# Optimization experiments

Measured on AMD Instinct MI355X. Metric: run time of the kernel, lower is better.

Reference implementation:

```python
import jax, jax.numpy as jnp
import numpy as np

B, NP, K = 8, 512, 64   # graphs, points per graph, knn neighbors
N = B * NP              # total nodes
EPS = 1e-5


def knn_edges(pos):
    """knn_graph(pos, k=K, batch, loop=True): edges (src=j neighbor, dst=i)."""
    p = pos.reshape(B, NP, 3)
    d2 = jnp.sum((p[:, :, None, :] - p[:, None, :, :]) ** 2, axis=-1)  # [B,NP,NP]
    _, idx = jax.lax.top_k(-d2, K)  # [B,NP,K] nearest (self included, d2=0)
    off = (jnp.arange(B, dtype=jnp.int32) * NP)[:, None, None]
    src = (idx.astype(jnp.int32) + off).reshape(-1)
    dst = jnp.broadcast_to(jnp.arange(NP, dtype=jnp.int32)[None, :, None] + off,
                           (B, NP, K)).reshape(-1)
    return src, dst


def graph_norm(x, batch, w, b, ms):
    """PyG GraphNorm: per-graph mean/std with learnable mean scale."""
    cnt = jax.ops.segment_sum(jnp.ones((x.shape[0], 1), x.dtype), batch, B)
    mean = jax.ops.segment_sum(x, batch, B) / cnt
    out = x - mean[batch] * ms
    var = jax.ops.segment_sum(out * out, batch, B) / cnt
    return w * out / jnp.sqrt(var + EPS)[batch] + b


def pointnet_layer(h, pos, src, dst, w1, b1, w2, b2):
    """message = MLP(concat(h_j, pos_j - pos_i)); aggregate = scatter-max over dst."""
    m = jnp.concatenate([h[src], pos[src] - pos[dst]], axis=-1)  # [E, Cin+3]
    m = jax.nn.relu(m @ w1 + b1) @ w2 + b2                        # [E, Cout]
    return jax.ops.segment_max(m, dst, N)


def _forward(batch, pos,
             gn1_w, gn1_b, gn1_ms, gn2_w, gn2_b, gn2_ms, gn3_w, gn3_b, gn3_ms,
             gn4_w, gn4_b, gn4_ms, gn5_w, gn5_b, gn5_ms, gn6_w, gn6_b, gn6_ms,
             c1_w1, c1_b1, c1_w2, c1_b2, c2_w1, c2_b1, c2_w2, c2_b2,
             c3_w1, c3_b1, c3_w2, c3_b2, c4_w1, c4_b1, c4_w2, c4_b2,
             c5_w1, c5_b1, c5_w2, c5_b2, cls_w, cls_b):
    src, dst = knn_edges(pos)
    h = graph_norm(pos, batch, gn1_w, gn1_b, gn1_ms)
    h = pointnet_layer(h, pos, src, dst, c1_w1, c1_b1, c1_w2, c1_b2)
    h = jax.nn.relu(graph_norm(h, batch, gn2_w, gn2_b, gn2_ms))
    h = pointnet_layer(h, pos, src, dst, c2_w1, c2_b1, c2_w2, c2_b2)
    h = jax.nn.relu(graph_norm(h, batch, gn3_w, gn3_b, gn3_ms))
    h = pointnet_layer(h, pos, src, dst, c3_w1, c3_b1, c3_w2, c3_b2)
    h = jax.nn.relu(graph_norm(h, batch, gn4_w, gn4_b, gn4_ms))
    h = pointnet_layer(h, pos, src, dst, c4_w1, c4_b1, c4_w2, c4_b2)
    h = jax.nn.relu(graph_norm(h, batch, gn5_w, gn5_b, gn5_ms))
    h = pointnet_layer(h, pos, src, dst, c5_w1, c5_b1, c5_w2, c5_b2)
    h = jax.nn.relu(graph_norm(h, batch, gn6_w, gn6_b, gn6_ms))
    return h @ cls_w + cls_b  # [N, 14]


def setup_inputs() -> dict:
    key = jax.random.key(0)
    ks = iter(jax.random.split(key, 40))
    inp = {}
    inp["pos"] = jax.random.normal(next(ks), (N, 3), jnp.float32)
    inp["batch"] = jnp.repeat(jnp.arange(B, dtype=jnp.int32), NP)
    for i, c in enumerate([3, 64, 128, 256, 512, 512], 1):
        inp[f"gn{i}_w"] = jnp.ones((c,), jnp.float32)
        inp[f"gn{i}_b"] = jnp.zeros((c,), jnp.float32)
        inp[f"gn{i}_ms"] = jnp.ones((c,), jnp.float32)
    for i, (ci, co) in enumerate([(3, 64), (64, 128), (128, 256), (256, 512), (512, 512)], 1):
        fin = ci + 3
        inp[f"c{i}_w1"] = jax.random.normal(next(ks), (fin, co), jnp.float32) / np.sqrt(fin).astype(np.float32)
        inp[f"c{i}_b1"] = jnp.zeros((co,), jnp.float32)
        inp[f"c{i}_w2"] = jax.random.normal(next(ks), (co, co), jnp.float32) / np.sqrt(co).astype(np.float32)
        inp[f"c{i}_b2"] = jnp.zeros((co,), jnp.float32)
    inp["cls_w"] = jax.random.normal(next(ks), (512, 14), jnp.float32) / np.float32(np.sqrt(512))
    inp["cls_b"] = jnp.zeros((14,), jnp.float32)
    return inp


def reference(pos, batch,
              gn1_w, gn1_b, gn1_ms, gn2_w, gn2_b, gn2_ms, gn3_w, gn3_b, gn3_ms,
              gn4_w, gn4_b, gn4_ms, gn5_w, gn5_b, gn5_ms, gn6_w, gn6_b, gn6_ms,
              c1_w1, c1_b1, c1_w2, c1_b2, c2_w1, c2_b1, c2_w2, c2_b2,
              c3_w1, c3_b1, c3_w2, c3_b2, c4_w1, c4_b1, c4_w2, c4_b2,
              c5_w1, c5_b1, c5_w2, c5_b2, cls_w, cls_b):
    return _forward(batch, pos,
                    gn1_w, gn1_b, gn1_ms, gn2_w, gn2_b, gn2_ms, gn3_w, gn3_b, gn3_ms,
                    gn4_w, gn4_b, gn4_ms, gn5_w, gn5_b, gn5_ms, gn6_w, gn6_b, gn6_ms,
                    c1_w1, c1_b1, c1_w2, c1_b2, c2_w1, c2_b1, c2_w2, c2_b2,
                    c3_w1, c3_b1, c3_w2, c3_b2, c4_w1, c4_b1, c4_w2, c4_b2,
                    c5_w1, c5_b1, c5_w2, c5_b2, cls_w, cls_b)
```

## Files before the change

kernel.cpp:

```cpp
#include <hip/hip_runtime.h>
#include <stdint.h>

#define N_NODES 4096
#define NGRAPH 8
#define NPTS 512
#define KNN 64
#define EPSN 1e-5f

typedef _Float16 f16x8 __attribute__((ext_vector_type(8)));
typedef float f32x4 __attribute__((ext_vector_type(4)));
typedef unsigned long long u64;

__device__ __forceinline__ unsigned short f2h(float f) {
    _Float16 h = (_Float16)f;
    union { _Float16 h; unsigned short u; } cv; cv.h = h;
    return cv.u;
}

__device__ __forceinline__ void w2cv(const float* __restrict__ src, unsigned short* __restrict__ dst,
                                     int off, int lg2c) {
    int C = 1 << lg2c;
    int k = off >> lg2c, n = off & (C - 1);
    int d = ((n >> 4) * (C / 32) + (k >> 5)) * 512 + ((k >> 3) & 3) * 128 + (n & 15) * 8 + (k & 7);
    dst[d] = f2h(src[off]);
}

__global__ __launch_bounds__(64) void setup_kernel(const float* __restrict__ pos, int* __restrict__ knn_out,
                                                   const float* __restrict__ wa, const float* __restrict__ wb,
                                                   const float* __restrict__ wc, const float* __restrict__ wd,
                                                   const float* __restrict__ we,
                                                   unsigned short* __restrict__ oa, unsigned short* __restrict__ ob,
                                                   unsigned short* __restrict__ oc, unsigned short* __restrict__ od,
                                                   unsigned short* __restrict__ oe,
                                                   float* __restrict__ statz,
                                                   const float* __restrict__ ms1, const float* __restrict__ gw1,
                                                   float* __restrict__ Aa, float* __restrict__ Sa) {
#pragma clang fp contract(off)
    __shared__ float px[NPTS], py[NPTS], pz[NPTS];
    __shared__ u64 keys[NPTS];
    int bid = blockIdx.x;
    int tid = threadIdx.x;
    int gidx = bid * 64 + tid;
    for (int idx = gidx; idx < 40960; idx += 262144) statz[idx] = 0.f;
    for (int idx = gidx; idx < 610304; idx += 262144) {
        if (idx < 4096)        w2cv(wa, oa, idx, 6);
        else if (idx < 20480)  w2cv(wb, ob, idx - 4096, 7);
        else if (idx < 86016)  w2cv(wc, oc, idx - 20480, 8);
        else if (idx < 348160) w2cv(wd, od, idx - 86016, 9);
        else                   w2cv(we, oe, idx - 348160, 9);
    }
    if (bid < 24) {
        int g = bid / 3, ch = bid - g * 3;
        float s1 = 0.f, s2 = 0.f;
        for (int n = tid; n < NPTS; n += 64) {
            float v = pos[(g * NPTS + n) * 3 + ch];
            s1 += v; s2 += v * v;
        }
        #pragma unroll
        for (int off = 32; off; off >>= 1) { s1 += __shfl_xor(s1, off); s2 += __shfl_xor(s2, off); }
        if (tid == 0) {
            float mean = s1 * (1.f / NPTS);
            float av = mean * ms1[ch];
            float var = s2 * (1.f / NPTS) - 2.f * av * mean + av * av;
            Aa[g * 3 + ch] = av;
            Sa[g * 3 + ch] = gw1[ch] / sqrtf(var + EPSN);
        }
    }
    int b = bid >> 9;
    int il = bid & (NPTS - 1);
    for (int n = tid; n < NPTS; n += 64) {
        int base = (b * NPTS + n) * 3;
        px[n] = pos[base]; py[n] = pos[base + 1]; pz[n] = pos[base + 2];
    }
    __syncthreads();
    float xi = px[il], yi = py[il], zi = pz[il];
    for (int n = tid; n < NPTS; n += 64) {
        float dx = px[n] - xi, dy = py[n] - yi, dz = pz[n] - zi;
        float d2 = dx * dx;
        d2 = d2 + dy * dy;
        d2 = d2 + dz * dz;
        keys[n] = (((u64)__float_as_uint(d2)) << 32) | (unsigned)n;
    }
    __syncthreads();
    for (int k2 = 2; k2 <= NPTS; k2 <<= 1) {
        for (int j = k2 >> 1; j > 0; j >>= 1) {
            #pragma unroll 4
            for (int p = 0; p < 4; ++p) {
                int pid = tid + p * 64;
                int t = ((pid & ~(j - 1)) << 1) | (pid & (j - 1));
                int ixj = t | j;
                u64 a = keys[t], c = keys[ixj];
                bool up = ((t & k2) == 0);
                if ((a > c) == up) { keys[t] = c; keys[ixj] = a; }
            }
            __syncthreads();
        }
    }
    int j0 = (int)(keys[tid] & 0xffffffffu);
    knn_out[(size_t)(b * NPTS + il) * KNN + tid] = b * NPTS + j0;
}

template<int CIN, int C, int RELU, int RAW>
__global__ __launch_bounds__(C) void node_kernel(const float* __restrict__ y, const float* __restrict__ pos,
                                                 const float* __restrict__ p1, const float* __restrict__ p2,
                                                 const float* __restrict__ ms, const float* __restrict__ gw,
                                                 const float* __restrict__ bnp,
                                                 const float* __restrict__ w1, const float* __restrict__ b1,
                                                 float* __restrict__ U, float* __restrict__ P) {
    constexpr int ROWS = 16;
    constexpr int KC = 64;
    constexpr int LDH = KC + 4;
    __shared__ float hs[ROWS][LDH];
    __shared__ float As_[CIN > 0 ? CIN : 1], Ss_[CIN > 0 ? CIN : 1];
    const int c = threadIdx.x;
    const int n0 = blockIdx.x * ROWS;
    const int b = n0 >> 9;
    if (RAW) {
        for (int ch = c; ch < CIN; ch += C) {
            float s1 = p1[b * CIN + ch], s2 = p2[b * CIN + ch];
            float mean = s1 * (1.f / NPTS);
            float a = mean * ms[ch];
            float var = s2 * (1.f / NPTS) - 2.f * a * mean + a * a;
            As_[ch] = a;
            Ss_[ch] = gw[ch] / sqrtf(var + EPSN);
        }
    }
    float acc[ROWS];
    #pragma unroll
    for (int r = 0; r < ROWS; ++r) acc[r] = 0.f;
    constexpr int NCHUNK = (CIN + KC - 1) / KC;
    #pragma unroll 1
    for (int s = 0; s < NCHUNK; ++s) {
        const int k0 = s * KC;
        const int kc = (CIN - k0 < KC) ? (CIN - k0) : KC;
        __syncthreads();
        for (int idx = c; idx < ROWS * kc; idx += C) {
            int r = idx / kc, k = idx - r * kc;
            int ch = k0 + k;
            float a = RAW ? As_[ch] : p1[b * CIN + ch];
            float sf = RAW ? Ss_[ch] : p2[b * CIN + ch];
            float v = (y[(size_t)(n0 + r) * CIN + ch] - a) * sf + bnp[ch];
            if (RELU) v = fmaxf(v, 0.f);
            hs[r][k] = v;
        }
        __syncthreads();
        int k = 0;
        for (; k + 4 <= kc; k += 4) {
            float w0 = w1[(size_t)(k0 + k) * C + c];
            float w1v = w1[(size_t)(k0 + k + 1) * C + c];
            float w2v = w1[(size_t)(k0 + k + 2) * C + c];
            float w3v = w1[(size_t)(k0 + k + 3) * C + c];
            #pragma unroll
            for (int r = 0; r < ROWS; ++r) {
                f32x4 hv = *(const f32x4*)&hs[r][k];
                acc[r] = fmaf(hv[0], w0, acc[r]);
                acc[r] = fmaf(hv[1], w1v, acc[r]);
                acc[r] = fmaf(hv[2], w2v, acc[r]);
                acc[r] = fmaf(hv[3], w3v, acc[r]);
            }
        }
        for (; k < kc; ++k) {
            float wv = w1[(size_t)(k0 + k) * C + c];
            #pragma unroll
            for (int r = 0; r < ROWS; ++r)
                acc[r] = fmaf(hs[r][k], wv, acc[r]);
        }
    }
    float pacc[ROWS];
    #pragma unroll
    for (int r = 0; r < ROWS; ++r) pacc[r] = 0.f;
    #pragma unroll
    for (int e = 0; e < 3; ++e) {
        float wv = w1[(size_t)(CIN + e) * C + c];
        #pragma unroll
        for (int r = 0; r < ROWS; ++r)
            pacc[r] = fmaf(pos[(n0 + r) * 3 + e], wv, pacc[r]);
    }
    float bv = b1[c];
    #pragma unroll
    for (int r = 0; r < ROWS; ++r) {
        U[(size_t)(n0 + r) * C + c] = acc[r] + pacc[r] + bv;
        P[(size_t)(n0 + r) * C + c] = pacc[r];
    }
}

template<int C, int W>
__global__ __launch_bounds__(W * 64, 4) void edge_kernel(const float* __restrict__ U, const float* __restrict__ P,
                                                         const int* __restrict__ knn, const unsigned short* __restrict__ w2t,
                                                         const float* __restrict__ b2, float* __restrict__ Y,
                                                         float* __restrict__ sum1, float* __restrict__ sum2) {
    constexpr int NCT = C / (W * 16);
    constexpr int EPT = 32 / W;
    constexpr int S = C / 32;
    constexpr int LD = 40;
    __shared__ unsigned short Tb[2][64 * LD];
    __shared__ int jn[64];
    const int bid = blockIdx.x;
    const int i = ((bid & 7) << 9) | (bid >> 3);
    const int tid = threadIdx.x;
    const int wave = tid >> 6, lane = tid & 63, m = lane & 15, quad = lane >> 4;
    const int cw = wave * (NCT * 16);
    if (tid < 64) jn[tid] = knn[(size_t)i * KNN + tid];
    f32x4 acc[4][NCT];
    f32x4 zero = {0.f, 0.f, 0.f, 0.f};
    #pragma unroll
    for (int rt = 0; rt < 4; ++rt)
        #pragma unroll
        for (int ct = 0; ct < NCT; ++ct)
            acc[rt][ct] = zero;
    const int rr = tid / W;
    const int c0 = (tid % W) * EPT;
    __syncthreads();
    const float* upr = U + (size_t)jn[rr] * C + c0;
    const float* ppr = P + (size_t)i * C + c0;
    float4 uf[EPT / 4], pf[EPT / 4];
    #pragma unroll
    for (int g = 0; g < EPT / 4; ++g) {
        uf[g] = *(const float4*)(upr + g * 4);
        pf[g] = *(const float4*)(ppr + g * 4);
    }
    #pragma unroll 2
    for (int s = 0; s < S; ++s) {
        unsigned short* tb = Tb[s & 1];
        if constexpr (EPT == 8) {
            uint4 pk;
            pk.x = (unsigned)f2h(fmaxf(uf[0].x - pf[0].x, 0.f)) | ((unsigned)f2h(fmaxf(uf[0].y - pf[0].y, 0.f)) << 16);
            pk.y = (unsigned)f2h(fmaxf(uf[0].z - pf[0].z, 0.f)) | ((unsigned)f2h(fmaxf(uf[0].w - pf[0].w, 0.f)) << 16);
            pk.z = (unsigned)f2h(fmaxf(uf[1].x - pf[1].x, 0.f)) | ((unsigned)f2h(fmaxf(uf[1].y - pf[1].y, 0.f)) << 16);
            pk.w = (unsigned)f2h(fmaxf(uf[1].z - pf[1].z, 0.f)) | ((unsigned)f2h(fmaxf(uf[1].w - pf[1].w, 0.f)) << 16);
            *(uint4*)&tb[rr * LD + c0] = pk;
        } else {
            uint2 pk;
            pk.x = (unsigned)f2h(fmaxf(uf[0].x - pf[0].x, 0.f)) | ((unsigned)f2h(fmaxf(uf[0].y - pf[0].y, 0.f)) << 16);
            pk.y = (unsigned)f2h(fmaxf(uf[0].z - pf[0].z, 0.f)) | ((unsigned)f2h(fmaxf(uf[0].w - pf[0].w, 0.f)) << 16);
            *(uint2*)&tb[rr * LD + c0] = pk;
        }
        if (s + 1 < S) {
            #pragma unroll
            for (int g = 0; g < EPT / 4; ++g) {
                uf[g] = *(const float4*)(upr + (s + 1) * 32 + g * 4);
                pf[g] = *(const float4*)(ppr + (s + 1) * 32 + g * 4);
            }
        }
        __syncthreads();
        f16x8 a[4];
        #pragma unroll
        for (int rt = 0; rt < 4; ++rt)
            a[rt] = *(const f16x8*)&tb[(rt * 16 + m) * LD + quad * 8];
        #pragma unroll
        for (int ct = 0; ct < NCT; ++ct) {
            const f16x8 bb = *(const f16x8*)(w2t +
                (size_t)(((cw >> 4) + ct) * S + s) * 512 + quad * 128 + m * 8);
            #pragma unroll
            for (int rt = 0; rt < 4; ++rt)
                acc[rt][ct] = __builtin_amdgcn_mfma_f32_16x16x32_f16(a[rt], bb, acc[rt][ct], 0, 0, 0);
        }
    }
    const int gb = i >> 9;
    #pragma unroll
    for (int ct = 0; ct < NCT; ++ct) {
        float vmax = -3.4e38f;
        #pragma unroll
        for (int rt = 0; rt < 4; ++rt) {
            vmax = fmaxf(vmax, acc[rt][ct][0]);
            vmax = fmaxf(vmax, acc[rt][ct][1]);
            vmax = fmaxf(vmax, acc[rt][ct][2]);
            vmax = fmaxf(vmax, acc[rt][ct][3]);
        }
        vmax = fmaxf(vmax, __shfl_xor(vmax, 16));
        vmax = fmaxf(vmax, __shfl_xor(vmax, 32));
        if (quad == 0) {
            int col = cw + ct * 16 + m;
            float val = vmax + b2[col];
            Y[(size_t)i * C + col] = val;
            atomicAdd(&sum1[gb * C + col], val);
            atomicAdd(&sum2[gb * C + col], val * val);
        }
    }
}

__global__ __launch_bounds__(256) void cls_kernel(const float* __restrict__ y, const float* __restrict__ sum1,
                                                  const float* __restrict__ sum2, const float* __restrict__ ms,
                                                  const float* __restrict__ gw, const float* __restrict__ gnb,
                                                  const float* __restrict__ w, const float* __restrict__ bias,
                                                  float* __restrict__ out) {
    __shared__ float wl[512 * 14];
    __shared__ _Float16 hn[16][520];
    __shared__ float As[512], Ss[512];
    int tid = threadIdx.x;
    int n0 = blockIdx.x * 16;
    int b = n0 >> 9;
    for (int ch = tid; ch < 512; ch += 256) {
        float s1 = sum1[b * 512 + ch], s2 = sum2[b * 512 + ch];
        float mean = s1 * (1.f / NPTS);
        float a = mean * ms[ch];
        float var = s2 * (1.f / NPTS) - 2.f * a * mean + a * a;
        As[ch] = a;
        Ss[ch] = gw[ch] / sqrtf(var + EPSN);
    }
    for (int idx = tid; idx < 512 * 14; idx += 256) wl[idx] = w[idx];
    __syncthreads();
    for (int idx = tid; idx < 16 * 512; idx += 256) {
        int r = idx >> 9, k = idx & 511;
        float v = (y[(size_t)(n0 + r) * 512 + k] - As[k]) * Ss[k] + gnb[k];
        hn[r][k] = (_Float16)fmaxf(v, 0.f);
    }
    __syncthreads();
    if (tid < 224) {
        int nl = tid / 14, c = tid - nl * 14;
        float acc = bias[c];
        for (int k = 0; k < 512; ++k)
            acc += (float)hn[nl][k] * wl[k * 14 + c];
        out[(size_t)(n0 + nl) * 14 + c] = acc;
    }
}

extern "C" void kernel_launch(void* const* d_in, const int* in_sizes, int n_in,
                              void* d_out, int out_size, void* d_ws, size_t ws_size,
                              hipStream_t stream) {
    const float* pos = (const float*)d_in[0];
    const float* gnw[6]; const float* gnb[6]; const float* gnms[6];
    for (int i = 0; i < 6; ++i) {
        gnw[i]  = (const float*)d_in[2 + 3 * i];
        gnb[i]  = (const float*)d_in[3 + 3 * i];
        gnms[i] = (const float*)d_in[4 + 3 * i];
    }
    const float* cw1[5]; const float* cb1[5]; const float* cw2[5]; const float* cb2[5];
    for (int i = 0; i < 5; ++i) {
        cw1[i] = (const float*)d_in[20 + 4 * i];
        cb1[i] = (const float*)d_in[21 + 4 * i];
        cw2[i] = (const float*)d_in[22 + 4 * i];
        cb2[i] = (const float*)d_in[23 + 4 * i];
    }
    const float* clsw = (const float*)d_in[40];
    const float* clsb = (const float*)d_in[41];
    float* out = (float*)d_out;

    char* ws = (char*)d_ws;
    int* knn             = (int*)(ws + 0);
    float* U             = (float*)(ws + 1048576);
    float* P             = (float*)(ws + 9437184);
    float* y             = (float*)(ws + 26214400);
    float* Aa            = (float*)(ws + 34603008);
    float* Sa            = (float*)(ws + 34619392);
    unsigned short* w2t0 = (unsigned short*)(ws + 34635776);
    unsigned short* w2t1 = (unsigned short*)(ws + 34643968);
    unsigned short* w2t2 = (unsigned short*)(ws + 34676736);
    unsigned short* w2t3 = (unsigned short*)(ws + 34807808);
    unsigned short* w2t4 = (unsigned short*)(ws + 35332096);
    float* acc           = (float*)(ws + 35856384);
    float* s1l[5]; float* s2l[5];
    for (int l = 0; l < 5; ++l) { s1l[l] = acc + l * 8192; s2l[l] = s1l[l] + 4096; }

    setup_kernel<<<N_NODES, 64, 0, stream>>>(pos, knn, cw2[0], cw2[1], cw2[2], cw2[3], cw2[4],
                                             w2t0, w2t1, w2t2, w2t3, w2t4, acc,
                                             gnms[0], gnw[0], Aa, Sa);

    node_kernel<3, 64, 0, 0><<<N_NODES / 16, 64, 0, stream>>>(pos, pos, Aa, Sa, gnms[0], gnw[0], gnb[0], cw1[0], cb1[0], U, P);
    edge_kernel<64, 4><<<N_NODES, 256, 0, stream>>>(U, P, knn, w2t0, cb2[0], y, s1l[0], s2l[0]);

    node_kernel<64, 128, 1, 1><<<N_NODES / 16, 128, 0, stream>>>(y, pos, s1l[0], s2l[0], gnms[1], gnw[1], gnb[1], cw1[1], cb1[1], U, P);
    edge_kernel<128, 8><<<N_NODES, 512, 0, stream>>>(U, P, knn, w2t1, cb2[1], y, s1l[1], s2l[1]);

    node_kernel<128, 256, 1, 1><<<N_NODES / 16, 256, 0, stream>>>(y, pos, s1l[1], s2l[1], gnms[2], gnw[2], gnb[2], cw1[2], cb1[2], U, P);
    edge_kernel<256, 8><<<N_NODES, 512, 0, stream>>>(U, P, knn, w2t2, cb2[2], y, s1l[2], s2l[2]);

    node_kernel<256, 512, 1, 1><<<N_NODES / 16, 512, 0, stream>>>(y, pos, s1l[2], s2l[2], gnms[3], gnw[3], gnb[3], cw1[3], cb1[3], U, P);
    edge_kernel<512, 8><<<N_NODES, 512, 0, stream>>>(U, P, knn, w2t3, cb2[3], y, s1l[3], s2l[3]);

    node_kernel<512, 512, 1, 1><<<N_NODES / 16, 512, 0, stream>>>(y, pos, s1l[3], s2l[3], gnms[4], gnw[4], gnb[4], cw1[4], cb1[4], U, P);
    edge_kernel<512, 8><<<N_NODES, 512, 0, stream>>>(U, P, knn, w2t4, cb2[4], y, s1l[4], s2l[4]);

    cls_kernel<<<N_NODES / 16, 256, 0, stream>>>(y, s1l[4], s2l[4], gnms[5], gnw[5], gnb[5], clsw, clsb, out);
}
```

Measured before the change: 749.2 us.

## Use 32x32x16 MFMA edge kernel with matching weight layout for wide layers

Adds an edge kernel built on 32x32x16 f16 MFMA tiles for the 256- and 512-channel layers, with a new swizzled weight layout produced in setup. It stages the relu(U_j - P_i) tile in double-buffered LDS in 32-wide K chunks and reduces the max over the 32-row accumulators. Larger MFMA tiles are meant to cut instruction count and LDS or global weight reads per FLOP. In exchange, the 16-float accumulators raise register pressure under launch bounds of 512 threads with 4 blocks per CU.

```diff
diff --git a/kernel.cpp b/kernel.cpp
--- a/kernel.cpp
+++ b/kernel.cpp
@@ -9,6 +9,7 @@
 
 typedef _Float16 f16x8 __attribute__((ext_vector_type(8)));
 typedef float f32x4 __attribute__((ext_vector_type(4)));
+typedef float f32x16 __attribute__((ext_vector_type(16)));
 typedef unsigned long long u64;
 
 __device__ __forceinline__ unsigned short f2h(float f) {
@@ -22,6 +23,13 @@
     int C = 1 << lg2c;
     int k = off >> lg2c, n = off & (C - 1);
     int d = ((n >> 4) * (C / 32) + (k >> 5)) * 512 + ((k >> 3) & 3) * 128 + (n & 15) * 8 + (k & 7);
+    dst[d] = f2h(src[off]);
+}
+__device__ __forceinline__ void w2cv32(const float* __restrict__ src, unsigned short* __restrict__ dst,
+                                       int off, int lg2c) {
+    int C = 1 << lg2c;
+    int k = off >> lg2c, n = off & (C - 1);
+    int d = ((n >> 5) * (C / 16) + (k >> 4)) * 512 + ((k >> 3) & 1) * 256 + (n & 31) * 8 + (k & 7);
     dst[d] = f2h(src[off]);
 }
 
@@ -45,9 +53,9 @@
     for (int idx = gidx; idx < 610304; idx += 262144) {
         if (idx < 4096)        w2cv(wa, oa, idx, 6);
         else if (idx < 20480)  w2cv(wb, ob, idx - 4096, 7);
-        else if (idx < 86016)  w2cv(wc, oc, idx - 20480, 8);
-        else if (idx < 348160) w2cv(wd, od, idx - 86016, 9);
-        else                   w2cv(we, oe, idx - 348160, 9);
+        else if (idx < 86016)  w2cv32(wc, oc, idx - 20480, 8);
+        else if (idx < 348160) w2cv32(wd, od, idx - 86016, 9);
+        else                   w2cv32(we, oe, idx - 348160, 9);
     }
     if (bid < 24) {
         int g = bid / 3, ch = bid - g * 3;
@@ -279,6 +287,89 @@
     }
 }
 
+template<int C>
+__global__ __launch_bounds__(512, 4) void edge_kernel32(const float* __restrict__ U, const float* __restrict__ P,
+                                                        const int* __restrict__ knn, const unsigned short* __restrict__ w2t,
+                                                        const float* __restrict__ b2, float* __restrict__ Y,
+                                                        float* __restrict__ sum1, float* __restrict__ sum2) {
+    constexpr int NCT = C / 256;
+    constexpr int S = C / 32;
+    constexpr int LD = 40;
+    __shared__ unsigned short Tb[2][64 * LD];
+    __shared__ int jn[64];
+    const int bid = blockIdx.x;
+    const int i = ((bid & 7) << 9) | (bid >> 3);
+    const int tid = threadIdx.x;
+    const int wave = tid >> 6, lane = tid & 63;
+    const int l31 = lane & 31, kh = lane >> 5;
+    const int ctb = wave * NCT;
+    if (tid < 64) jn[tid] = knn[(size_t)i * KNN + tid];
+    f32x16 acc[2][NCT];
+    #pragma unroll
+    for (int rt = 0; rt < 2; ++rt)
+        #pragma unroll
+        for (int ct = 0; ct < NCT; ++ct)
+            #pragma unroll
+            for (int e = 0; e < 16; ++e)
+                acc[rt][ct][e] = 0.f;
+    const int rr = tid >> 3;
+    const int c0 = (tid & 7) * 4;
+    __syncthreads();
+    const float* upr = U + (size_t)jn[rr] * C + c0;
+    const float* ppr = P + (size_t)i * C + c0;
+    const unsigned short* wb = w2t + kh * 256 + l31 * 8;
+    float4 uf = *(const float4*)upr;
+    float4 pf = *(const float4*)ppr;
+    #pragma unroll 2
+    for (int s = 0; s < S; ++s) {
+        unsigned short* tb = Tb[s & 1];
+        uint2 pk;
+        pk.x = (unsigned)f2h(fmaxf(uf.x - pf.x, 0.f)) | ((unsigned)f2h(fmaxf(uf.y - pf.y, 0.f)) << 16);
+        pk.y = (unsigned)f2h(fmaxf(uf.z - pf.z, 0.f)) | ((unsigned)f2h(fmaxf(uf.w - pf.w, 0.f)) << 16);
+        *(uint2*)&tb[rr * LD + c0] = pk;
+        if (s + 1 < S) {
+            uf = *(const float4*)(upr + (s + 1) * 32);
+            pf = *(const float4*)(ppr + (s + 1) * 32);
+        }
+        __syncthreads();
+        f16x8 a[2][2];
+        #pragma unroll
+        for (int rt = 0; rt < 2; ++rt)
+            #pragma unroll
+            for (int kk = 0; kk < 2; ++kk)
+                a[rt][kk] = *(const f16x8*)&tb[(rt * 32 + l31) * LD + kk * 16 + kh * 8];
+        #pragma unroll
+        for (int ct = 0; ct < NCT; ++ct) {
+            #pragma unroll
+            for (int kk = 0; kk < 2; ++kk) {
+                const f16x8 bb = *(const f16x8*)(wb +
+                    (size_t)((ctb + ct) * (C / 16) + (s * 2 + kk)) * 512);
+                #pragma unroll
+                for (int rt = 0; rt < 2; ++rt)
+                    acc[rt][ct] = __builtin_amdgcn_mfma_f32_32x32x16_f16(a[rt][kk], bb, acc[rt][ct], 0, 0, 0);
+            }
+        }
+    }
+    const int gb = i >> 9;
+    #pragma unroll
+    for (int ct = 0; ct < NCT; ++ct) {
+        float vmax = -3.4e38f;
+        #pragma unroll
+        for (int rt = 0; rt < 2; ++rt)
+            #pragma unroll
+            for (int r = 0; r < 16; ++r)
+                vmax = fmaxf(vmax, acc[rt][ct][r]);
+        vmax = fmaxf(vmax, __shfl_xor(vmax, 32));
+        if (kh == 0) {
+            int col = (ctb + ct) * 32 + l31;
+            float val = vmax + b2[col];
+            Y[(size_t)i * C + col] = val;
+            atomicAdd(&sum1[gb * C + col], val);
+            atomicAdd(&sum2[gb * C + col], val * val);
+        }
+    }
+}
+
 __global__ __launch_bounds__(256) void cls_kernel(const float* __restrict__ y, const float* __restrict__ sum1,
                                                   const float* __restrict__ sum2, const float* __restrict__ ms,
                                                   const float* __restrict__ gw, const float* __restrict__ gnb,
@@ -363,13 +454,13 @@
     edge_kernel<128, 8><<<N_NODES, 512, 0, stream>>>(U, P, knn, w2t1, cb2[1], y, s1l[1], s2l[1]);
 
     node_kernel<128, 256, 1, 1><<<N_NODES / 16, 256, 0, stream>>>(y, pos, s1l[1], s2l[1], gnms[2], gnw[2], gnb[2], cw1[2], cb1[2], U, P);
-    edge_kernel<256, 8><<<N_NODES, 512, 0, stream>>>(U, P, knn, w2t2, cb2[2], y, s1l[2], s2l[2]);
+    edge_kernel32<256><<<N_NODES, 512, 0, stream>>>(U, P, knn, w2t2, cb2[2], y, s1l[2], s2l[2]);
 
     node_kernel<256, 512, 1, 1><<<N_NODES / 16, 512, 0, stream>>>(y, pos, s1l[2], s2l[2], gnms[3], gnw[3], gnb[3], cw1[3], cb1[3], U, P);
-    edge_kernel<512, 8><<<N_NODES, 512, 0, stream>>>(U, P, knn, w2t3, cb2[3], y, s1l[3], s2l[3]);
+    edge_kernel32<512><<<N_NODES, 512, 0, stream>>>(U, P, knn, w2t3, cb2[3], y, s1l[3], s2l[3]);
 
     node_kernel<512, 512, 1, 1><<<N_NODES / 16, 512, 0, stream>>>(y, pos, s1l[3], s2l[3], gnms[4], gnw[4], gnb[4], cw1[4], cb1[4], U, P);
-    edge_kernel<512, 8><<<N_NODES, 512, 0, stream>>>(U, P, knn, w2t4, cb2[4], y, s1l[4], s2l[4]);
+    edge_kernel32<512><<<N_NODES, 512, 0, stream>>>(U, P, knn, w2t4, cb2[4], y, s1l[4], s2l[4]);
 
     cls_kernel<<<N_NODES / 16, 256, 0, stream>>>(y, s1l[4], s2l[4], gnms[5], gnw[5], gnb[5], clsw, clsb, out);
 }
```

New measurement: 759.2 us. About the same (+1.3%).
